# Performance work log

Hardware: AMD Instinct MI355X
Metric: run time of the kernel (lower is better)

Reference implementation:

```python
import jax, jax.numpy as jnp
import numpy as np

LEAKY = 0.1
U, I, D, H, L, E = 100000, 50000, 128, 128, 2, 1600000


def setup_inputs() -> dict:
    key = jax.random.key(0)
    ks = jax.random.split(key, 11)
    s = 1.0 / np.sqrt(D)
    return {
        "uEmbed0": jax.random.normal(ks[0], (U, D), jnp.float32) * s,
        "iEmbed0": jax.random.normal(ks[1], (I, D), jnp.float32) * s,
        "uhyper": jax.random.normal(ks[2], (D, H), jnp.float32) * s,
        "ihyper": jax.random.normal(ks[3], (D, H), jnp.float32) * s,
        "vals": jax.random.uniform(ks[4], (E,), jnp.float32),
        "hgnn_u_W": jax.random.normal(ks[5], (L, 3, H, H), jnp.float32) * (1.0 / np.sqrt(H)),
        "hgnn_i_W": jax.random.normal(ks[6], (L, 3, H, H), jnp.float32) * (1.0 / np.sqrt(H)),
        "gcn_u_W": jax.random.normal(ks[7], (L, D, D), jnp.float32) * s,
        "gcn_i_W": jax.random.normal(ks[8], (L, D, D), jnp.float32) * s,
        "rows": jax.random.randint(ks[9], (E,), 0, U, jnp.int32),
        "cols": jax.random.randint(ks[10], (E,), 0, I, jnp.int32),
    }


def reference(uEmbed0, iEmbed0, uhyper, ihyper, vals, hgnn_u_W, hgnn_i_W, gcn_u_W, gcn_i_W, rows, cols):
    nU, nI = uEmbed0.shape[0], iEmbed0.shape[0]

    def lrelu(x):
        return jax.nn.leaky_relu(x, LEAKY)

    # sparse adjacency (COO) matvecs: adj [nU, nI], adj.T [nI, nU]
    def spmm_u(x):  # adj @ x -> [nU, d]
        return jax.ops.segment_sum(vals[:, None] * x[cols], rows, num_segments=nU)

    def spmm_i(x):  # adj.T @ x -> [nI, d]
        return jax.ops.segment_sum(vals[:, None] * x[rows], cols, num_segments=nI)

    def hgnn(lats, adj, Ws):  # adj: [N, H] dense hyper adjacency, lats: [N, d]
        lat = lrelu(adj.T @ lats)            # [H, d]
        for w in Ws:                         # 3 residual FC blocks on transposed lat
            lat = jax.nn.relu(lat.T @ w).T + lat
        return lrelu(adj @ lat)              # [N, d]

    uuHyper = uEmbed0 @ uhyper  # [nU, H]
    iiHyper = iEmbed0 @ ihyper  # [nI, H]

    ulat, ilat = uEmbed0, iEmbed0
    uSum, iSum = uEmbed0, iEmbed0
    for l in range(hgnn_u_W.shape[0]):
        hU = hgnn(ulat, uuHyper, hgnn_u_W[l])
        hI = hgnn(ilat, iiHyper, hgnn_i_W[l])
        gU = lrelu(jax.nn.relu(spmm_u(ilat) @ gcn_u_W[l]))  # GCNLayer: leaky(relu((adj@lats)@W))
        gI = lrelu(jax.nn.relu(spmm_i(ulat) @ gcn_i_W[l]))
        ulat = gU + hU + ulat
        ilat = gI + hI + ilat
        uSum = uSum + ulat
        iSum = iSum + ilat
    return uSum, iSum
```

## Files before the change

### kernel.cpp

```cpp
#include <hip/hip_runtime.h>
#include <stdint.h>

#define LEAKY 0.1f
typedef unsigned short u16;
typedef unsigned int u32;
typedef unsigned char u8;
typedef short bf16x8 __attribute__((ext_vector_type(8)));
typedef float f32x4 __attribute__((ext_vector_type(4)));
typedef float f32x2 __attribute__((ext_vector_type(2)));

__device__ __forceinline__ float bflo(u32 u){ union{u32 i; float f;} c; c.i = u<<16; return c.f; }
__device__ __forceinline__ float bfhi(u32 u){ union{u32 i; float f;} c; c.i = u & 0xffff0000u; return c.f; }
__device__ __forceinline__ float bf2f(u16 v){ union{u32 i; float f;} c; c.i = ((u32)v)<<16; return c.f; }
__device__ __forceinline__ u16 f2bf(float f){
  union{float f; u32 i;} c; c.f = f;
  u32 r = (c.i + 0x7fffu + ((c.i>>16)&1u)) >> 16;
  return (u16)r;
}
__device__ __forceinline__ u32 pack2(float a, float b){ return (u32)f2bf(a) | ((u32)f2bf(b)<<16); }

__device__ __forceinline__ u32 f2fp8(float f){
  union{float f; u32 i;} c; c.f = f;
  u32 s = (c.i >> 24) & 0x80u;
  float a = fabsf(f); if (a > 448.f) a = 448.f;
  union{float f; u32 i;} d; d.f = a * 0x1p-120f;
  u32 u = d.i;
  u32 r = (u + 0x7FFFFu + ((u >> 20) & 1u)) >> 20;
  if (r > 0x7Eu) r = 0x7Eu;
  return s | r;
}
__device__ __forceinline__ f32x2 fp8x2_to_f(u32 b2){
  return __builtin_amdgcn_cvt_pk_f32_fp8((int)b2, false);
}

__device__ __forceinline__ void load8f(const float* p, float* v){
  const float4* q = (const float4*)p; float4 a = q[0], b = q[1];
  v[0]=a.x;v[1]=a.y;v[2]=a.z;v[3]=a.w;v[4]=b.x;v[5]=b.y;v[6]=b.z;v[7]=b.w;
}
__device__ __forceinline__ void load8h(const u16* p, float* v){
  uint4 u = *(const uint4*)p;
  v[0]=bflo(u.x);v[1]=bfhi(u.x);v[2]=bflo(u.y);v[3]=bfhi(u.y);
  v[4]=bflo(u.z);v[5]=bfhi(u.z);v[6]=bflo(u.w);v[7]=bfhi(u.w);
}
__device__ __forceinline__ void load4f(const float* p, float* v){
  float4 a = *(const float4*)p; v[0]=a.x;v[1]=a.y;v[2]=a.z;v[3]=a.w;
}
__device__ __forceinline__ void load4h(const u16* p, float* v){
  uint2 u = *(const uint2*)p;
  v[0]=bflo(u.x); v[1]=bfhi(u.x); v[2]=bflo(u.y); v[3]=bfhi(u.y);
}
__device__ __forceinline__ void store2bf(u16* p, float a, float b){
  *(u32*)p = pack2(a,b);
}
__device__ __forceinline__ void store4bf(u16* p, float a, float b, float c, float d){
  uint2 t; t.x = pack2(a,b); t.y = pack2(c,d);
  *(uint2*)p = t;
}

__global__ __launch_bounds__(256) void zero_kernel(int* p, int n){
  int i = blockIdx.x*256 + threadIdx.x;
  if (i < n) p[i] = 0;
}

__device__ __forceinline__ void stageWt(const float* __restrict__ W, u16* Wt, int tid){
  const int n = tid & 127, khalf = tid >> 7;
#pragma unroll
  for (int g = 0; g < 16; ++g) {
    int k0 = khalf*64 + g*4;
    float w0 = W[(k0+0)*128 + n];
    float w1 = W[(k0+1)*128 + n];
    float w2 = W[(k0+2)*128 + n];
    float w3 = W[(k0+3)*128 + n];
    uint2 t; t.x = pack2(w0,w1); t.y = pack2(w2,w3);
    *(uint2*)&Wt[n*136 + k0] = t;
  }
}

__device__ __forceinline__ void gemm_core(
    const float* __restrict__ Af, const u16* __restrict__ Ah,
    const float* __restrict__ W, u16* __restrict__ C, u8* __restrict__ C8,
    int N, int brow, u16* Wt, int tid)
{
  stageWt(W, Wt, tid);
  __syncthreads();

  const int w = tid >> 6, lane = tid & 63;
  const int m = lane & 15, quad = lane >> 4;
  const int rowBase = brow*64 + w*16;
  int arow = rowBase + m;
  if (arow >= N) arow = N-1;

  bf16x8 af[4];
  if (Ah) {
#pragma unroll
    for (int kt=0; kt<4; ++kt)
      af[kt] = *(const bf16x8*)(Ah + (size_t)arow*128 + kt*32 + quad*8);
  } else {
#pragma unroll
    for (int kt=0; kt<4; ++kt) {
      float v[8]; load8f(Af + (size_t)arow*128 + kt*32 + quad*8, v);
      bf16x8 t;
#pragma unroll
      for (int j=0;j<8;++j) t[j] = (short)f2bf(v[j]);
      af[kt] = t;
    }
  }

#pragma unroll
  for (int jt=0; jt<8; ++jt) {
    f32x4 acc = {0.f,0.f,0.f,0.f};
#pragma unroll
    for (int kt=0; kt<4; ++kt) {
      bf16x8 bf = *(const bf16x8*)&Wt[(jt*16+m)*136 + kt*32 + quad*8];
      acc = __builtin_amdgcn_mfma_f32_16x16x32_bf16(af[kt], bf, acc, 0, 0, 0);
    }
    const int col = jt*16 + m;
#pragma unroll
    for (int r=0;r<4;++r) {
      int rg = rowBase + quad*4 + r;
      if (rg < N) {
        if (C8) C8[(size_t)rg*128 + col] = (u8)f2fp8(acc[r]);
        else    C[(size_t)rg*128 + col] = f2bf(acc[r]);
      }
    }
  }
}

__global__ __launch_bounds__(256) void gemm128_dual(
    const float* Af1, const u16* Ah1, const float* W1, u16* C1, u8* C81, int N1, int g1,
    const float* Af2, const u16* Ah2, const float* W2, u16* C2, u8* C82, int N2)
{
  __shared__ alignas(16) u16 Wt[128*136];
  const int b = blockIdx.x;
  if (b < g1) gemm_core(Af1, Ah1, W1, C1, C81, N1, b,      Wt, threadIdx.x);
  else        gemm_core(Af2, Ah2, W2, C2, C82, N2, b - g1, Wt, threadIdx.x);
}

__global__ __launch_bounds__(256) void update_dual(
    const u16* T1, const u16* Hy1, const float* W1,
    const float* PF1, const u16* PH1, u16* Po1, float* S1, const float* B1, int N1, int g1,
    const u16* T2, const u16* Hy2, const float* W2,
    const float* PF2, const u16* PH2, u16* Po2, float* S2, const float* B2, int N2, int smode)
{
  __shared__ alignas(16) char shmem[34816];
  u16* Wt = (u16*)shmem;
  float* Gs = (float*)shmem;
  const int tid = threadIdx.x;
  const int b = blockIdx.x;

  const u16* T; const u16* Hy; const float* latW;
  const float* PrevF; const u16* PrevH; u16* Pout; float* S; const float* B; int N; int brow;
  if (b < g1) { T=T1; Hy=Hy1; latW=W1; PrevF=PF1; PrevH=PH1; Pout=Po1; S=S1; B=B1; N=N1; brow=b; }
  else        { T=T2; Hy=Hy2; latW=W2; PrevF=PF2; PrevH=PH2; Pout=Po2; S=S2; B=B2; N=N2; brow=b-g1; }

  stageWt(latW, Wt, tid);
  __syncthreads();

  const int w = tid >> 6, lane = tid & 63;
  const int m = lane & 15, quad = lane >> 4;
  const int rowBase = brow*64;
  int arow = rowBase + w*16 + m;
  if (arow >= N) arow = N-1;

  bf16x8 af[4];
#pragma unroll
  for (int kt=0; kt<4; ++kt)
    af[kt] = *(const bf16x8*)(Hy + (size_t)arow*128 + kt*32 + quad*8);

  f32x4 acc[8];
#pragma unroll
  for (int jt=0; jt<8; ++jt) {
    f32x4 a = {0.f,0.f,0.f,0.f};
#pragma unroll
    for (int kt=0; kt<4; ++kt) {
      bf16x8 bf = *(const bf16x8*)&Wt[(jt*16+m)*136 + kt*32 + quad*8];
      a = __builtin_amdgcn_mfma_f32_16x16x32_bf16(af[kt], bf, a, 0, 0, 0);
    }
    acc[jt] = a;
  }
  __syncthreads();
#pragma unroll
  for (int jt=0; jt<8; ++jt) {
#pragma unroll
    for (int r=0;r<4;++r) {
      float x = acc[jt][r];
      Gs[(w*16 + quad*4 + r)*132 + jt*16 + m] = x > 0.f ? x : LEAKY*x;
    }
  }
  __syncthreads();

  const int c4 = (tid & 31) * 4;
  const int r0 = tid >> 5;
#pragma unroll
  for (int ri=0; ri<8; ++ri) {
    int lr = r0 + ri*8;
    int n = rowBase + lr;
    if (n >= N) continue;
    size_t off = (size_t)n*128 + c4;
    float gv[4]; load4f(&Gs[lr*132 + c4], gv);
    float tv[4], pv[4], ov[4];
    load4h(T + off, tv);
    if (PrevH) load4h(PrevH + off, pv);
    else       load4f(PrevF + off, pv);
#pragma unroll
    for (int cc=0;cc<4;++cc) ov[cc] = gv[cc] + tv[cc] + pv[cc];
    if (Pout)
      store4bf(&Pout[off], ov[0],ov[1],ov[2],ov[3]);
    if (smode == 0) {
      float4 s = *(const float4*)&S[off];
      s.x += ov[0]; s.y += ov[1]; s.z += ov[2]; s.w += ov[3];
      *(float4*)&S[off] = s;
    } else if (smode == 1) {
      float4 s; s.x=pv[0]+ov[0]; s.y=pv[1]+ov[1]; s.z=pv[2]+ov[2]; s.w=pv[3]+ov[3];
      *(float4*)&S[off] = s;
    } else if (smode == 3) {
      float bv[4]; load4f(B + off, bv);
      float4 s; s.x=bv[0]+pv[0]+ov[0]; s.y=bv[1]+pv[1]+ov[1];
      s.z=bv[2]+pv[2]+ov[2]; s.w=bv[3]+pv[3]+ov[3];
      *(float4*)&S[off] = s;
    }
  }
}

#define RPAD 40
__global__ __launch_bounds__(256) void reduce_kernel(
    const u16* __restrict__ HyU, const u16* __restrict__ HyI,
    const float* __restrict__ LatUf, const u16* __restrict__ LatUh,
    const float* __restrict__ LatIf, const u16* __restrict__ LatIh,
    u16* __restrict__ part, int Nu, int Ni, int nbU)
{
  __shared__ alignas(16) u16 HsT[128*RPAD];
  __shared__ alignas(16) u16 LsT[128*RPAD];
  const int b = blockIdx.x;
  const u16* Hy; const float* Lf; const u16* Lh; int N, cstart;
  if (b < nbU) { Hy=HyU; Lf=LatUf; Lh=LatUh; N=Nu; cstart = b*256; }
  else         { Hy=HyI; Lf=LatIf; Lh=LatIh; N=Ni; cstart = (b-nbU)*256; }
  const int cend = (N < cstart+256) ? N : (cstart+256);
  const int tid = threadIdx.x;
  const int w = tid >> 6, lane = tid & 63;
  const int m = lane & 15, quad = lane >> 4;

  f32x4 acc[2][8];
#pragma unroll
  for (int a=0;a<2;++a)
#pragma unroll
    for (int c=0;c<8;++c) { acc[a][c][0]=0.f; acc[a][c][1]=0.f; acc[a][c][2]=0.f; acc[a][c][3]=0.f; }

  for (int t0 = cstart; t0 < cend; t0 += 32) {
#pragma unroll
    for (int it=0; it<2; ++it) {
      const int idx = it*256 + tid;
      const int n = idx & 31, h0 = (idx >> 5) * 8;
      const int row = t0 + n;
      u32 ax=0, ay=0, az=0, aw=0, lx=0, ly=0, lz=0, lw=0;
      if (row < cend) {
        uint4 uh = *(const uint4*)(Hy + (size_t)row*128 + h0);
        ax=uh.x; ay=uh.y; az=uh.z; aw=uh.w;
        if (Lh) {
          uint4 ul = *(const uint4*)(Lh + (size_t)row*128 + h0);
          lx=ul.x; ly=ul.y; lz=ul.z; lw=ul.w;
        } else {
          float v[8]; load8f(Lf + (size_t)row*128 + h0, v);
          lx = pack2(v[0],v[1]); ly = pack2(v[2],v[3]);
          lz = pack2(v[4],v[5]); lw = pack2(v[6],v[7]);
        }
      }
      u16* hp = &HsT[h0*RPAD + n];
      hp[0*RPAD]=(u16)ax; hp[1*RPAD]=(u16)(ax>>16);
      hp[2*RPAD]=(u16)ay; hp[3*RPAD]=(u16)(ay>>16);
      hp[4*RPAD]=(u16)az; hp[5*RPAD]=(u16)(az>>16);
      hp[6*RPAD]=(u16)aw; hp[7*RPAD]=(u16)(aw>>16);
      u16* lp = &LsT[h0*RPAD + n];
      lp[0*RPAD]=(u16)lx; lp[1*RPAD]=(u16)(lx>>16);
      lp[2*RPAD]=(u16)ly; lp[3*RPAD]=(u16)(ly>>16);
      lp[4*RPAD]=(u16)lz; lp[5*RPAD]=(u16)(lz>>16);
      lp[6*RPAD]=(u16)lw; lp[7*RPAD]=(u16)(lw>>16);
    }
    __syncthreads();
    bf16x8 a0 = *(const bf16x8*)&HsT[(w*32 +      m)*RPAD + quad*8];
    bf16x8 a1 = *(const bf16x8*)&HsT[(w*32 + 16 + m)*RPAD + quad*8];
#pragma unroll
    for (int td=0; td<8; ++td) {
      bf16x8 bfr = *(const bf16x8*)&LsT[(td*16 + m)*RPAD + quad*8];
      acc[0][td] = __builtin_amdgcn_mfma_f32_16x16x32_bf16(a0, bfr, acc[0][td], 0, 0, 0);
      acc[1][td] = __builtin_amdgcn_mfma_f32_16x16x32_bf16(a1, bfr, acc[1][td], 0, 0, 0);
    }
    __syncthreads();
  }
  u16* pb = part + (size_t)b*16384;
#pragma unroll
  for (int th=0; th<2; ++th) {
    const int h = w*32 + th*16 + quad*4;
#pragma unroll
    for (int td=0; td<8; ++td) {
      const int d = td*16 + m;
#pragma unroll
      for (int r=0;r<4;++r)
        pb[(size_t)(h+r)*128 + d] = f2bf(acc[th][td][r]);
    }
  }
}

#define JS 16
__global__ __launch_bounds__(256) void reduce2a_kernel(
    const u16* __restrict__ part, float* __restrict__ Rp,
    int nbU, int nbI)
{
  const int e = blockIdx.x*256 + threadIdx.x;
  const int side = blockIdx.z;
  const int nb = side ? nbI : nbU;
  const int per = (nb + JS - 1) / JS;
  const int j0 = blockIdx.y * per;
  int j1 = j0 + per; if (j1 > nb) j1 = nb;
  const u16* p = part + (side ? (size_t)nbU*16384 : 0) + e;
  float s = 0.f;
  for (int j=j0; j<j1; ++j) s += bf2f(p[(size_t)j*16384]);
  Rp[((size_t)side*JS + blockIdx.y)*16384 + e] = s;
}

__global__ __launch_bounds__(256) void reduce2b_kernel(
    const float* __restrict__ Rp, float* __restrict__ Ru, float* __restrict__ Ri)
{
  const int e = blockIdx.x*256 + threadIdx.x;
  const int side = blockIdx.y;
  const float* p = Rp + (size_t)side*JS*16384 + e;
  float s = 0.f;
#pragma unroll
  for (int j=0; j<JS; ++j) s += p[(size_t)j*16384];
  if (side) Ri[e] = s; else Ru[e] = s;
}

__global__ __launch_bounds__(128) void fc_kernel(
    const float* __restrict__ Ru, const float* __restrict__ Ri,
    const float* __restrict__ W3u, const float* __restrict__ W3i,
    float* __restrict__ latU, float* __restrict__ latI)
{
  __shared__ float cur[128];
  const int h = threadIdx.x;
  const int d = blockIdx.x;
  const int side = blockIdx.y;
  const float* R  = side ? Ri  : Ru;
  const float* W3 = side ? W3i : W3u;
  float* lat      = side ? latI : latU;
  float x = R[h*128 + d];
  cur[h] = x > 0.f ? x : LEAKY*x;
  __syncthreads();
  for (int s=0;s<3;++s) {
    const float* w = W3 + s*16384 + h;
    float val = 0.f;
#pragma unroll 8
    for (int hp=0; hp<128; ++hp) val = fmaf(cur[hp], w[hp*128], val);
    val = (val > 0.f ? val : 0.f) + cur[h];
    __syncthreads();
    cur[h] = val;
    __syncthreads();
  }
  lat[h*128+d] = cur[h];
}

__global__ __launch_bounds__(256) void spmm_kernel(
    const uint2* __restrict__ csr, const int* __restrict__ rowptr,
    const u8* __restrict__ Y, u16* __restrict__ T, int N, int Ncol, int E)
{
  const int lane = threadIdx.x & 63;
  const int row = blockIdx.x*4 + (threadIdx.x >> 6);
  if (row >= N) return;
  int e  = rowptr[row];
  int e1 = rowptr[row+1];
  if (e < 0) e = 0;
  if (e > E) e = E;
  if (e1 < e) e1 = e;
  if (e1 > E) e1 = E;
  const u32 cmax = (u32)(Ncol - 1);
  float a0=0.f, a1=0.f;
  const int c2 = lane*2;
  for (; e+4 <= e1; e += 4) {
    uint2 p0 = csr[e], p1 = csr[e+1], p2 = csr[e+2], p3 = csr[e+3];
    u32 i0 = p0.x < cmax ? p0.x : cmax;
    u32 i1 = p1.x < cmax ? p1.x : cmax;
    u32 i2 = p2.x < cmax ? p2.x : cmax;
    u32 i3 = p3.x < cmax ? p3.x : cmax;
    u32 y0 = *(const u16*)&Y[(size_t)i0*128 + c2];
    u32 y1 = *(const u16*)&Y[(size_t)i1*128 + c2];
    u32 y2 = *(const u16*)&Y[(size_t)i2*128 + c2];
    u32 y3 = *(const u16*)&Y[(size_t)i3*128 + c2];
    float v0 = __uint_as_float(p0.y), v1 = __uint_as_float(p1.y);
    float v2 = __uint_as_float(p2.y), v3 = __uint_as_float(p3.y);
    f32x2 d0 = fp8x2_to_f(y0), d1 = fp8x2_to_f(y1);
    f32x2 d2 = fp8x2_to_f(y2), d3 = fp8x2_to_f(y3);
    a0 = fmaf(v0, d0[0], a0); a1 = fmaf(v0, d0[1], a1);
    a0 = fmaf(v1, d1[0], a0); a1 = fmaf(v1, d1[1], a1);
    a0 = fmaf(v2, d2[0], a0); a1 = fmaf(v2, d2[1], a1);
    a0 = fmaf(v3, d3[0], a0); a1 = fmaf(v3, d3[1], a1);
  }
  for (; e < e1; ++e) {
    uint2 p0 = csr[e];
    u32 i0 = p0.x < cmax ? p0.x : cmax;
    u32 y0 = *(const u16*)&Y[(size_t)i0*128 + c2];
    float v0 = __uint_as_float(p0.y);
    f32x2 d0 = fp8x2_to_f(y0);
    a0 = fmaf(v0, d0[0], a0); a1 = fmaf(v0, d0[1], a1);
  }
  store2bf(&T[(size_t)row*128 + c2], a0 > 0.f ? a0 : 0.f, a1 > 0.f ? a1 : 0.f);
}

#define HCB 32768
#define HWORDS (HCB/2)
#define HS  64
__global__ __launch_bounds__(256) void hist_part_kernel(
    const int* __restrict__ rows, const int* __restrict__ cols,
    u32* __restrict__ part, int E, int cU)
{
  __shared__ alignas(16) u32 h[HWORDS];
  const int c = blockIdx.x, s = blockIdx.y;
  const int* key = (c < cU) ? rows : cols;
  const u32 lo = (u32)((c < cU ? c : c - cU) * HCB);
  {
    uint4 z; z.x=0; z.y=0; z.z=0; z.w=0;
    uint4* h4 = (uint4*)h;
    for (int i = threadIdx.x; i < HWORDS/4; i += 256) h4[i] = z;
  }
  __syncthreads();
  int per = (E + HS - 1) / HS;
  per = (per + 3) & ~3;
  const int e0 = s*per;
  const int e1 = (E < e0+per) ? E : (e0+per);
  if (e0 < e1) {
    const int4* kp = (const int4*)(key + e0);
    const int nv = (e1 - e0) >> 2;
    for (int i = threadIdx.x; i < nv; i += 256) {
      int4 kv = kp[i];
      u32 k0=(u32)kv.x-lo, k1=(u32)kv.y-lo, k2=(u32)kv.z-lo, k3=(u32)kv.w-lo;
      if (k0 < (u32)HCB) atomicAdd(&h[k0>>1], 1u << ((k0&1)<<4));
      if (k1 < (u32)HCB) atomicAdd(&h[k1>>1], 1u << ((k1&1)<<4));
      if (k2 < (u32)HCB) atomicAdd(&h[k2>>1], 1u << ((k2&1)<<4));
      if (k3 < (u32)HCB) atomicAdd(&h[k3>>1], 1u << ((k3&1)<<4));
    }
    for (int e = e0 + (nv<<2) + threadIdx.x; e < e1; e += 256) {
      u32 k = (u32)key[e] - lo;
      if (k < (u32)HCB) atomicAdd(&h[k>>1], 1u << ((k&1)<<4));
    }
  }
  __syncthreads();
  uint4* dst = (uint4*)(part + (size_t)(c*HS + s) * HWORDS);
  const uint4* h4 = (const uint4*)h;
  for (int i = threadIdx.x; i < HWORDS/4; i += 256) dst[i] = h4[i];
}

__global__ __launch_bounds__(256) void scan_local_kernel(
    const u32* __restrict__ part,
    int* rpU, int* rpI, int* bsU, int* bsI, int Nu, int Ni, int cU)
{
  const int side = blockIdx.y;
  const int Nn = side ? Ni : Nu;
  int* rp = side ? rpI : rpU;
  int* bs = side ? bsI : bsU;
  const int nb = (Nn + 4095) >> 12;
  if ((int)blockIdx.x >= nb) return;
  __shared__ int sa[256], sb[256];
  const int tid = threadIdx.x;
  const int base = blockIdx.x*4096 + tid*16;
  int v[16];
#pragma unroll
  for (int q=0;q<16;++q) v[q]=0;
  {
    const int gc = (side ? cU : 0) + (base >> 15);
    const int w0 = (base & (HCB-1)) >> 1;
    const u32* ps = part + (size_t)gc*HS*HWORDS + w0;
    for (int s=0; s<HS; ++s) {
      const uint4* pw = (const uint4*)(ps + (size_t)s*HWORDS);
      uint4 a = pw[0], b = pw[1];
      v[0]+= (int)(a.x&0xffffu); v[1]+= (int)(a.x>>16);
      v[2]+= (int)(a.y&0xffffu); v[3]+= (int)(a.y>>16);
      v[4]+= (int)(a.z&0xffffu); v[5]+= (int)(a.z>>16);
      v[6]+= (int)(a.w&0xffffu); v[7]+= (int)(a.w>>16);
      v[8]+= (int)(b.x&0xffffu); v[9]+= (int)(b.x>>16);
      v[10]+=(int)(b.y&0xffffu); v[11]+=(int)(b.y>>16);
      v[12]+=(int)(b.z&0xffffu); v[13]+=(int)(b.z>>16);
      v[14]+=(int)(b.w&0xffffu); v[15]+=(int)(b.w>>16);
    }
  }
  int sum = 0;
#pragma unroll
  for (int q=0;q<16;++q) sum += v[q];
  sa[tid] = sum; __syncthreads();
  int* src = sa; int* dst = sb;
  for (int off=1; off<256; off<<=1) {
    int x = src[tid] + ((tid>=off) ? src[tid-off] : 0);
    dst[tid] = x;
    __syncthreads();
    int* t = src; src = dst; dst = t;
  }
  const int incl = src[tid];
  int run = incl - sum;
#pragma unroll
  for (int q=0;q<16;++q){ int idx=base+q; if (idx<Nn) rp[idx]=run; run+=v[q]; }
  if (tid==255) bs[blockIdx.x] = incl;
}

__global__ void scan_blocks_kernel(int* bsU, int* bsI, int* rpU, int* rpI, int Nu, int Ni)
{
  if (threadIdx.x != 0) return;
  const int side = blockIdx.y;
  int* bs = side?bsI:bsU; int* rp = side?rpI:rpU;
  const int Nn = side?Ni:Nu;
  const int nb = (Nn+4095)>>12;
  int run = 0;
  for (int b=0;b<nb;++b){ int t=bs[b]; bs[b]=run; run+=t; }
  rp[Nn] = run;
}

__global__ __launch_bounds__(256) void scan_add_kernel(
    const int* bsU, const int* bsI, int* rpU, int* rpI, int Nu, int Ni)
{
  const int side = blockIdx.y;
  const int Nn = side?Ni:Nu;
  const int* bs = side?bsI:bsU;
  int* rp = side?rpI:rpU;
  const int nb = (Nn+4095)>>12;
  if ((int)blockIdx.x >= nb) return;
  const int add = bs[blockIdx.x];
  const int base = blockIdx.x*4096 + threadIdx.x*16;
#pragma unroll
  for (int q=0;q<16;++q){ int idx=base+q; if (idx<Nn) rp[idx]+=add; }
}

__global__ __launch_bounds__(256) void scatter_kernel(
    const int* __restrict__ rows, const int* __restrict__ cols, const float* __restrict__ vals,
    const int* __restrict__ rpU, const int* __restrict__ rpI,
    int* curU, int* curI, uint2* csrU, uint2* csrI, int E, int Nu, int Ni,
    int u0, int u1, int i0w, int i1w)
{
  (void)u0; (void)u1;
  int e = blockIdx.x*256 + threadIdx.x;
  if (e >= E) return;
  int r = rows[e], c = cols[e];
  if ((unsigned)r < (unsigned)Nu && (unsigned)c < (unsigned)Ni) {
    u32 vb = __float_as_uint(vals[e]);
    if (c >= i0w && c < i1w) {
      int su = rpU[r] + atomicAdd(&curU[r], 1);
      if ((unsigned)su < (unsigned)E) { uint2 t; t.x=(u32)c; t.y=vb; csrU[su]=t; }
      int si = rpI[c] + atomicAdd(&curI[c], 1);
      if ((unsigned)si < (unsigned)E) { uint2 t; t.x=(u32)r; t.y=vb; csrI[si]=t; }
    }
  }
}

extern "C" void kernel_launch(void* const* d_in, const int* in_sizes, int n_in,
                              void* d_out, int out_size, void* d_ws, size_t ws_size,
                              hipStream_t stream)
{
  const float* uE     = (const float*)d_in[0];
  const float* iE     = (const float*)d_in[1];
  const float* uhyper = (const float*)d_in[2];
  const float* ihyper = (const float*)d_in[3];
  const float* vals   = (const float*)d_in[4];
  const float* WhU    = (const float*)d_in[5];
  const float* WhI    = (const float*)d_in[6];
  const float* WgU    = (const float*)d_in[7];
  const float* WgI    = (const float*)d_in[8];
  const int*   rows   = (const int*)d_in[9];
  const int*   cols   = (const int*)d_in[10];
  const int U = in_sizes[0]/128;
  const int I = in_sizes[1]/128;
  const int E = in_sizes[4];
  const int L = in_sizes[7]/(128*128);
  (void)n_in; (void)out_size;

  float* Su = (float*)d_out;
  float* Si = Su + (size_t)U*128;

  char* base0 = (char*)d_ws;
  u16* uuH; u16* iiH; u16* PU; u16* PI; u16* YU; u16* TU; u16* pool3;
  uint2* csrU; uint2* csrI; int* rpU; int* rpI; int* cntU; int* cntI;
  int* bsU; int* bsI; float* Ru; float* Ri; float* latU; float* latI; float* Rp;
  {
    size_t off = 0;
    #define ALLOC(var, type, bytes) var = (type)(base0 + off); off = (off + (bytes) + 255) & ~(size_t)255;
    ALLOC(uuH,  u16*, (size_t)U*128*2)
    ALLOC(iiH,  u16*, (size_t)I*128*2)
    ALLOC(PU,   u16*, (size_t)U*128*2)
    ALLOC(PI,   u16*, (size_t)I*128*2)
    ALLOC(YU,   u16*, (size_t)U*128*2)
    ALLOC(TU,   u16*, (size_t)U*128*2)
    ALLOC(pool3,u16*, (size_t)I*128*2)
    ALLOC(csrU, uint2*, (size_t)E*8)
    ALLOC(csrI, uint2*, (size_t)E*8)
    ALLOC(rpU,  int*, (size_t)(U+1)*4)
    ALLOC(rpI,  int*, (size_t)(I+1)*4)
    ALLOC(cntU, int*, (size_t)U*4)
    ALLOC(cntI, int*, (size_t)I*4)
    ALLOC(bsU,  int*, 64*4)
    ALLOC(bsI,  int*, 64*4)
    ALLOC(Ru,   float*, 16384*4)
    ALLOC(Ri,   float*, 16384*4)
    ALLOC(latU, float*, 16384*4)
    ALLOC(latI, float*, 16384*4)
    ALLOC(Rp,   float*, (size_t)2*JS*16384*4)
    #undef ALLOC
    if (off > ws_size) return;
  }
  const int cntN = (int)(((size_t)((char*)bsU - (char*)cntU)) / 4);

  const int nbU = (U+4095)>>12, nbI = (I+4095)>>12;
  const int nbMax = nbU > nbI ? nbU : nbI;
  const int rbU = (U+255)>>8, rbI = (I+255)>>8;
  const int gU = (U+63)/64, gI = (I+63)/64;
  const int cU = (U + HCB-1)/HCB, cI = (I + HCB-1)/HCB;

  u32* hpart = (u32*)csrU;
  u8* Y8u = (u8*)YU;
  u8* Y8i = (u8*)pool3;

  hist_part_kernel<<<dim3(cU+cI, HS), 256, 0, stream>>>(rows, cols, hpart, E, cU);
  scan_local_kernel<<<dim3(nbMax,2), 256, 0, stream>>>(hpart,rpU,rpI,bsU,bsI,U,I,cU);
  scan_blocks_kernel<<<dim3(1,2), 64, 0, stream>>>(bsU,bsI,rpU,rpI,U,I);
  scan_add_kernel<<<dim3(nbMax,2), 256, 0, stream>>>(bsU,bsI,rpU,rpI,U,I);
  zero_kernel<<<(cntN+255)/256, 256, 0, stream>>>(cntU, cntN);
  for (int wnd = 0; wnd < 4; ++wnd) {
    int u0 = (int)(((long long)wnd   * U) / 4);
    int u1 = (int)(((long long)(wnd+1) * U) / 4);
    int i0w = (int)(((long long)wnd   * I) / 4);
    int i1w = (int)(((long long)(wnd+1) * I) / 4);
    scatter_kernel<<<(E+255)/256, 256, 0, stream>>>(
        rows, cols, vals, rpU, rpI, cntU, cntI, csrU, csrI, E, U, I,
        u0, u1, i0w, i1w);
  }

  gemm128_dual<<<gU+gI, 256, 0, stream>>>(uE, (const u16*)0, uhyper, uuH, (u8*)0, U, gU,
                                          iE, (const u16*)0, ihyper, iiH, (u8*)0, I);

  for (int l=0; l<L; ++l) {
    const float* wgu = WgU + (size_t)l*16384;
    const float* wgi = WgI + (size_t)l*16384;
    const float* whu = WhU + (size_t)l*3*16384;
    const float* whi = WhI + (size_t)l*3*16384;
    const bool last = (l == L-1);
    int smode;
    if (l == 0) smode = (L == 1) ? 1 : 2;
    else if (l == 1) smode = 3;
    else smode = 0;
    if (l == 0) {
      gemm128_dual<<<gI+gU, 256, 0, stream>>>(iE, (const u16*)0, wgu, (u16*)0, Y8i, I, gI,
                                              uE, (const u16*)0, wgi, (u16*)0, Y8u, U);
      spmm_kernel<<<(U+3)/4, 256, 0, stream>>>(csrU, rpU, Y8i, TU, U, I, E);
      spmm_kernel<<<(I+3)/4, 256, 0, stream>>>(csrI, rpI, Y8u, pool3, I, U, E);
      reduce_kernel<<<rbU+rbI, 256, 0, stream>>>(uuH,iiH, uE,(const u16*)0, iE,(const u16*)0, YU,U,I,rbU);
      reduce2a_kernel<<<dim3(64,JS,2), 256, 0, stream>>>(YU, Rp, rbU, rbI);
      reduce2b_kernel<<<dim3(64,2), 256, 0, stream>>>(Rp, Ru, Ri);
      fc_kernel<<<dim3(128,2), 128, 0, stream>>>(Ru,Ri,whu,whi,latU,latI);
      update_dual<<<gU+gI, 256, 0, stream>>>(
          TU,    uuH, latU, uE, (const u16*)0, PU, Su, uE, U, gU,
          pool3, iiH, latI, iE, (const u16*)0, PI, Si, iE, I, smode);
    } else {
      gemm128_dual<<<gI+gU, 256, 0, stream>>>((const float*)0, PI, wgu, (u16*)0, Y8i, I, gI,
                                              (const float*)0, PU, wgi, (u16*)0, Y8u, U);
      spmm_kernel<<<(U+3)/4, 256, 0, stream>>>(csrU, rpU, Y8i, TU, U, I, E);
      spmm_kernel<<<(I+3)/4, 256, 0, stream>>>(csrI, rpI, Y8u, pool3, I, U, E);
      reduce_kernel<<<rbU+rbI, 256, 0, stream>>>(uuH,iiH, (const float*)0,PU, (const float*)0,PI, YU,U,I,rbU);
      reduce2a_kernel<<<dim3(64,JS,2), 256, 0, stream>>>(YU, Rp, rbU, rbI);
      reduce2b_kernel<<<dim3(64,2), 256, 0, stream>>>(Rp, Ru, Ri);
      fc_kernel<<<dim3(128,2), 128, 0, stream>>>(Ru,Ri,whu,whi,latU,latI);
      update_dual<<<gU+gI, 256, 0, stream>>>(
          TU,    uuH, latU, (const float*)0, PU, last?(u16*)0:PU, Su, uE, U, gU,
          pool3, iiH, latI, (const float*)0, PI, last?(u16*)0:PI, Si, iE, I, smode);
    }
  }
}
```

Before: 861.3 us.

## Replace global-atomic COO-to-CSR scatter with chunked shared-memory histogram scatter

The four windowed scatter passes, which used global atomic counters per row and column, are replaced by a per-chunk prefix over the existing partitioned histograms followed by one scatter kernel. That kernel ranks edges with 16-bit packed shared-memory atomics inside each key chunk and edge slice. This removes the zeroing kernel, the global atomics and the repeated passes over the edge list. In exchange, every chunk block rescans its whole edge slice, and the histogram scratch moves from csrU to the uuH buffer.

After: 865.7 us. Within noise of the previous version (+0.5%).

```diff
diff --git a/kernel.cpp b/kernel.cpp
--- a/kernel.cpp
+++ b/kernel.cpp
@@ -55,11 +55,6 @@
 __device__ __forceinline__ void store4bf(u16* p, float a, float b, float c, float d){
   uint2 t; t.x = pack2(a,b); t.y = pack2(c,d);
   *(uint2*)p = t;
-}
-
-__global__ __launch_bounds__(256) void zero_kernel(int* p, int n){
-  int i = blockIdx.x*256 + threadIdx.x;
-  if (i < n) p[i] = 0;
 }
 
 __device__ __forceinline__ void stageWt(const float* __restrict__ W, u16* Wt, int tid){
@@ -525,23 +520,64 @@
   for (int q=0;q<16;++q){ int idx=base+q; if (idx<Nn) rp[idx]+=add; }
 }
 
-__global__ __launch_bounds__(256) void scatter_kernel(
+__global__ __launch_bounds__(256) void hist_prefix_kernel(u32* part, int nC)
+{
+  const int c = blockIdx.x;
+  const int w = blockIdx.y*256 + threadIdx.x;
+  if (c >= nC || w >= HWORDS) return;
+  u32* p = part + (size_t)c*HS*HWORDS + w;
+  u32 run = 0;
+  for (int s = 0; s < HS; ++s) {
+    u32 t = p[(size_t)s*HWORDS];
+    p[(size_t)s*HWORDS] = run;
+    run += t;
+  }
+}
+
+__global__ __launch_bounds__(256) void scatter_det_kernel(
     const int* __restrict__ rows, const int* __restrict__ cols, const float* __restrict__ vals,
     const int* __restrict__ rpU, const int* __restrict__ rpI,
-    int* curU, int* curI, uint2* csrU, uint2* csrI, int E, int Nu, int Ni,
-    int u0, int u1, int i0w, int i1w)
-{
-  (void)u0; (void)u1;
-  int e = blockIdx.x*256 + threadIdx.x;
-  if (e >= E) return;
-  int r = rows[e], c = cols[e];
-  if ((unsigned)r < (unsigned)Nu && (unsigned)c < (unsigned)Ni) {
-    u32 vb = __float_as_uint(vals[e]);
-    if (c >= i0w && c < i1w) {
-      int su = rpU[r] + atomicAdd(&curU[r], 1);
-      if ((unsigned)su < (unsigned)E) { uint2 t; t.x=(u32)c; t.y=vb; csrU[su]=t; }
-      int si = rpI[c] + atomicAdd(&curI[c], 1);
-      if ((unsigned)si < (unsigned)E) { uint2 t; t.x=(u32)r; t.y=vb; csrI[si]=t; }
+    const u32* __restrict__ pref,
+    uint2* __restrict__ csrU, uint2* __restrict__ csrI,
+    int E, int Nu, int Ni, int cU)
+{
+  __shared__ alignas(16) u32 h[HWORDS];
+  const int c = blockIdx.x, s = blockIdx.y;
+  {
+    uint4 z; z.x=0; z.y=0; z.z=0; z.w=0;
+    uint4* h4 = (uint4*)h;
+    for (int i = threadIdx.x; i < HWORDS/4; i += 256) h4[i] = z;
+  }
+  __syncthreads();
+  const bool isU = (c < cU);
+  const int* key = isU ? rows : cols;
+  const int* oth = isU ? cols : rows;
+  const int* rp  = isU ? rpU  : rpI;
+  const int Nk   = isU ? Nu : Ni;
+  const int No   = isU ? Ni : Nu;
+  uint2* csr     = isU ? csrU : csrI;
+  const u32 lo = (u32)((isU ? c : c - cU) * HCB);
+  const u32* pb = pref + (size_t)(c*HS + s) * HWORDS;
+  int per = (E + HS - 1) / HS;
+  per = (per + 3) & ~3;
+  const int e0 = s*per;
+  const int e1 = (E < e0+per) ? E : (e0+per);
+  for (int e = e0 + threadIdx.x; e < e1; e += 256) {
+    int kf = key[e];
+    u32 k = (u32)kf - lo;
+    if (k < (u32)HCB && (unsigned)kf < (unsigned)Nk) {
+      int o = oth[e];
+      if ((unsigned)o < (unsigned)No) {
+        const int sh = (int)((k & 1u) << 4);
+        u32 old = atomicAdd(&h[k>>1], 1u << sh);
+        u32 rank = (old >> sh) & 0xffffu;
+        u32 base = (pb[k>>1] >> sh) & 0xffffu;
+        int slot = rp[kf] + (int)base + (int)rank;
+        if ((unsigned)slot < (unsigned)E) {
+          uint2 t; t.x = (u32)o; t.y = __float_as_uint(vals[e]);
+          csr[slot] = t;
+        }
+      }
     }
   }
 }
@@ -572,7 +608,7 @@
 
   char* base0 = (char*)d_ws;
   u16* uuH; u16* iiH; u16* PU; u16* PI; u16* YU; u16* TU; u16* pool3;
-  uint2* csrU; uint2* csrI; int* rpU; int* rpI; int* cntU; int* cntI;
+  uint2* csrU; uint2* csrI; int* rpU; int* rpI;
   int* bsU; int* bsI; float* Ru; float* Ri; float* latU; float* latI; float* Rp;
   {
     size_t off = 0;
@@ -588,8 +624,6 @@
     ALLOC(csrI, uint2*, (size_t)E*8)
     ALLOC(rpU,  int*, (size_t)(U+1)*4)
     ALLOC(rpI,  int*, (size_t)(I+1)*4)
-    ALLOC(cntU, int*, (size_t)U*4)
-    ALLOC(cntI, int*, (size_t)I*4)
     ALLOC(bsU,  int*, 64*4)
     ALLOC(bsI,  int*, 64*4)
     ALLOC(Ru,   float*, 16384*4)
@@ -600,7 +634,6 @@
     #undef ALLOC
     if (off > ws_size) return;
   }
-  const int cntN = (int)(((size_t)((char*)bsU - (char*)cntU)) / 4);
 
   const int nbU = (U+4095)>>12, nbI = (I+4095)>>12;
   const int nbMax = nbU > nbI ? nbU : nbI;
@@ -608,7 +641,7 @@
   const int gU = (U+63)/64, gI = (I+63)/64;
   const int cU = (U + HCB-1)/HCB, cI = (I + HCB-1)/HCB;
 
-  u32* hpart = (u32*)csrU;
+  u32* hpart = (u32*)uuH;
   u8* Y8u = (u8*)YU;
   u8* Y8i = (u8*)pool3;
 
@@ -616,16 +649,9 @@
   scan_local_kernel<<<dim3(nbMax,2), 256, 0, stream>>>(hpart,rpU,rpI,bsU,bsI,U,I,cU);
   scan_blocks_kernel<<<dim3(1,2), 64, 0, stream>>>(bsU,bsI,rpU,rpI,U,I);
   scan_add_kernel<<<dim3(nbMax,2), 256, 0, stream>>>(bsU,bsI,rpU,rpI,U,I);
-  zero_kernel<<<(cntN+255)/256, 256, 0, stream>>>(cntU, cntN);
-  for (int wnd = 0; wnd < 4; ++wnd) {
-    int u0 = (int)(((long long)wnd   * U) / 4);
-    int u1 = (int)(((long long)(wnd+1) * U) / 4);
-    int i0w = (int)(((long long)wnd   * I) / 4);
-    int i1w = (int)(((long long)(wnd+1) * I) / 4);
-    scatter_kernel<<<(E+255)/256, 256, 0, stream>>>(
-        rows, cols, vals, rpU, rpI, cntU, cntI, csrU, csrI, E, U, I,
-        u0, u1, i0w, i1w);
-  }
+  hist_prefix_kernel<<<dim3(cU+cI, HWORDS/256), 256, 0, stream>>>(hpart, cU+cI);
+  scatter_det_kernel<<<dim3(cU+cI, HS), 256, 0, stream>>>(
+      rows, cols, vals, rpU, rpI, hpart, csrU, csrI, E, U, I, cU);
 
   gemm128_dual<<<gU+gI, 256, 0, stream>>>(uE, (const u16*)0, uhyper, uuH, (u8*)0, U, gU,
                                           iE, (const u16*)0, ihyper, iiH, (u8*)0, I);
```
